# Optimization experiments

Hardware: AMD Instinct MI355X
Metric: run time of the kernel (lower is better)

The kernel has to match this reference:

```python
import jax, jax.numpy as jnp
import numpy as np

N_NODES = 500000


def _gconv(x, src, dst, ew, w_neigh, b, w_self):
    # DGL GraphConv(norm='none'): multiply weight first (in>=out here), then aggregate.
    h = x @ w_neigh                      # [N, out]
    msg = h[src] * ew[:, None]           # [E, out]
    agg = jax.ops.segment_sum(msg, dst, num_segments=N_NODES)
    return agg + b + x @ w_self          # neigh conv (+bias) + self-loop linear (no bias)


def setup_inputs() -> dict:
    key = jax.random.key(0)
    ks = jax.random.split(key, 16)
    N, E, G, F = N_NODES, 16000000, 64, 16
    inp = {
        "x": jax.random.normal(ks[0], (N, F), jnp.float32),
        "src": jax.random.randint(ks[1], (E,), 0, N),
        "dst": jax.random.randint(ks[2], (E,), 0, N),
        "graph_id": jnp.sort(jax.random.randint(ks[3], (N,), 0, G)),
        "edge_weight": jax.random.uniform(ks[4], (E,), jnp.float32),
        "num_graphs": G,
        "w_neigh0": jax.random.normal(ks[5], (F, 1), jnp.float32),
        "b0": jax.random.normal(ks[6], (1,), jnp.float32),
        "w_self0": jax.random.normal(ks[7], (F, 1), jnp.float32),
        "w_neigh1": jax.random.normal(ks[8], (1, 1), jnp.float32),
        "b1": jax.random.normal(ks[9], (1,), jnp.float32),
        "w_self1": jax.random.normal(ks[10], (1, 1), jnp.float32),
        "w_neigh2": jax.random.normal(ks[11], (1, 1), jnp.float32),
        "b2": jax.random.normal(ks[12], (1,), jnp.float32),
        "w_self2": jax.random.normal(ks[13], (1, 1), jnp.float32),
        "fc1_w": jax.random.normal(ks[14], (8, 1), jnp.float32),
        "fc1_b": jax.random.normal(ks[15], (8,), jnp.float32),
        "out_w": jax.random.normal(jax.random.fold_in(key, 100), (4, 8), jnp.float32),
        "out_b": jax.random.normal(jax.random.fold_in(key, 101), (4,), jnp.float32),
    }
    return inp


def reference(x, src, dst, graph_id, edge_weight, num_graphs,
              w_neigh0, b0, w_self0, w_neigh1, b1, w_self1,
              w_neigh2, b2, w_self2, fc1_w, fc1_b, out_w, out_b):
    h = jax.nn.relu(_gconv(x, src, dst, edge_weight, w_neigh0, b0, w_self0))
    h = jax.nn.relu(_gconv(h, src, dst, edge_weight, w_neigh1, b1, w_self1))
    h = jax.nn.relu(_gconv(h, src, dst, edge_weight, w_neigh2, b2, w_self2))
    # dgl.sum_nodes: per-graph segment sum over batched graph -> [G, 1]
    hg = jax.ops.segment_sum(h, graph_id, num_segments=num_graphs)
    hg2 = jax.nn.sigmoid((hg @ fc1_w.T + fc1_b) * 1000.0)   # [G, 8]
    out = jax.nn.relu(hg2 @ out_w.T + out_b)                # [G, 4]
    return jax.nn.log_softmax(out, axis=1)
```

## Files before the change

kernel.cpp:

```cpp
#include <hip/hip_runtime.h>

#define N_NODES   500000
#define NGRAPH    64
#define FDIM      16
#define NPB       4096
#define NPB_SHIFT 12
#define NBINS     123
#define SLICES    4
#define NBLK      512
#define CH        4096
typedef unsigned int u32;
typedef unsigned long long u64;

__global__ void proj_kernel(const float* __restrict__ x,
                            const float* __restrict__ wn,
                            const float* __restrict__ wsf,
                            float* __restrict__ a,
                            float* __restrict__ s) {
    int i = blockIdx.x * blockDim.x + threadIdx.x;
    if (i >= N_NODES) return;
    const float4* xr = (const float4*)(x + (size_t)i * FDIM);
    float4 v0 = xr[0], v1 = xr[1], v2 = xr[2], v3 = xr[3];
    const float4* n4 = (const float4*)wn;
    const float4* s4 = (const float4*)wsf;
    float4 n0 = n4[0], n1 = n4[1], n2 = n4[2], n3 = n4[3];
    float4 w0 = s4[0], w1 = s4[1], w2 = s4[2], w3 = s4[3];
    float an = v0.x*n0.x + v0.y*n0.y + v0.z*n0.z + v0.w*n0.w
             + v1.x*n1.x + v1.y*n1.y + v1.z*n1.z + v1.w*n1.w
             + v2.x*n2.x + v2.y*n2.y + v2.z*n2.z + v2.w*n2.w
             + v3.x*n3.x + v3.y*n3.y + v3.z*n3.z + v3.w*n3.w;
    float as = v0.x*w0.x + v0.y*w0.y + v0.z*w0.z + v0.w*w0.w
             + v1.x*w1.x + v1.y*w1.y + v1.z*w1.z + v1.w*w1.w
             + v2.x*w2.x + v2.y*w2.y + v2.z*w2.z + v2.w*w2.w
             + v3.x*w3.x + v3.y*w3.y + v3.z*w3.z + v3.w*w3.w;
    a[i] = an;
    s[i] = as;
}

__global__ __launch_bounds__(1024) void hist_kernel(const int* __restrict__ dst, int E, int chunk,
                                                    u32* __restrict__ blockHist) {
    __shared__ u32 cnt[NBINS];
    for (int t = threadIdx.x; t < NBINS; t += 1024) cnt[t] = 0;
    __syncthreads();
    int b = blockIdx.x;
    int lo = b * chunk, hi = min(lo + chunk, E);
    int m = (hi - lo) & ~3;
    for (int i = lo + threadIdx.x * 4; i < lo + m; i += 4096) {
        int4 d = *(const int4*)(dst + i);
        atomicAdd(&cnt[((u32)d.x) >> NPB_SHIFT], 1u);
        atomicAdd(&cnt[((u32)d.y) >> NPB_SHIFT], 1u);
        atomicAdd(&cnt[((u32)d.z) >> NPB_SHIFT], 1u);
        atomicAdd(&cnt[((u32)d.w) >> NPB_SHIFT], 1u);
    }
    for (int i = lo + m + threadIdx.x; i < hi; i += 1024)
        atomicAdd(&cnt[((u32)dst[i]) >> NPB_SHIFT], 1u);
    __syncthreads();
    for (int t = threadIdx.x; t < NBINS; t += 1024)
        blockHist[(size_t)b * NBINS + t] = cnt[t];
}

__global__ __launch_bounds__(NBLK) void scan1_kernel(u32* __restrict__ blockHist,
                                                     u32* __restrict__ binTotal) {
    int j = blockIdx.x;
    __shared__ u32 lsum[NBLK];
    int t = threadIdx.x;
    u32 v = blockHist[(size_t)t * NBINS + j];
    lsum[t] = v;
    __syncthreads();
    u32 x = v;
    for (int off = 1; off < NBLK; off <<= 1) {
        u32 y = (t >= off) ? lsum[t - off] : 0u;
        __syncthreads();
        x += y; lsum[t] = x;
        __syncthreads();
    }
    if (t == NBLK - 1) binTotal[j] = x;
    blockHist[(size_t)t * NBINS + j] = x - v;
}

__global__ void scan2_kernel(const u32* __restrict__ binTotal, u32* __restrict__ binStart) {
    if (threadIdx.x == 0) {
        u32 run = 0;
        for (int j = 0; j < NBINS; ++j) { binStart[j] = run; run += binTotal[j]; }
        binStart[NBINS] = run;
    }
}

__global__ __launch_bounds__(512) void scatter_staged(const int* __restrict__ src,
                                                      const int* __restrict__ dst,
                                                      const float* __restrict__ ew,
                                                      int E, int chunk,
                                                      const u32* __restrict__ blockHist,
                                                      const u32* __restrict__ binStart,
                                                      u64* __restrict__ binned) {
    __shared__ u32 cursor[NBINS];
    __shared__ u32 cnt[NBINS];
    __shared__ u32 off[NBINS];
    __shared__ u64 stage[CH];
    __shared__ unsigned char binOf[CH];
    int b   = blockIdx.x;
    int tid = threadIdx.x;
    for (int t = tid; t < NBINS; t += 512)
        cursor[t] = binStart[t] + blockHist[(size_t)b * NBINS + t];
    int lo = b * chunk, hiB = min(lo + chunk, E);
    for (int base = lo; base < hiB; base += CH) {
        int n = min(CH, hiB - base);
        for (int t = tid; t < NBINS; t += 512) cnt[t] = 0;
        __syncthreads();
        u32 rec[8]; float wv[8]; u32 bi[8]; u32 rk[8];
#pragma unroll
        for (int k = 0; k < 8; ++k) {
            int idx = base + k * 512 + tid;
            bi[k] = 0xFFFFFFFFu;
            if (idx < base + n) {
                u32 d  = (u32)dst[idx];
                bi[k]  = d >> NPB_SHIFT;
                rec[k] = ((u32)src[idx]) | ((d & (NPB - 1)) << 19);
                wv[k]  = ew[idx];
                rk[k]  = atomicAdd(&cnt[bi[k]], 1u);
            }
        }
        __syncthreads();
        if (tid < NBINS) off[tid] = cnt[tid];
        __syncthreads();
        for (int d2 = 1; d2 < 128; d2 <<= 1) {
            u32 v = 0;
            if (tid < NBINS) { v = off[tid]; if (tid >= d2) v += off[tid - d2]; }
            __syncthreads();
            if (tid < NBINS) off[tid] = v;
            __syncthreads();
        }
        if (tid < NBINS) off[tid] -= cnt[tid];
        __syncthreads();
#pragma unroll
        for (int k = 0; k < 8; ++k) {
            if (bi[k] != 0xFFFFFFFFu) {
                u32 p = off[bi[k]] + rk[k];
                stage[p] = (u64)rec[k] | ((u64)__float_as_uint(wv[k]) << 32);
                binOf[p] = (unsigned char)bi[k];
            }
        }
        __syncthreads();
        for (int p = tid; p < n; p += 512) {
            u32 j = binOf[p];
            binned[cursor[j] + ((u32)p - off[j])] = stage[p];
        }
        __syncthreads();
        for (int t = tid; t < NBINS; t += 512) cursor[t] += cnt[t];
        __syncthreads();
    }
}

__global__ __launch_bounds__(512) void bin_pass(const u64* __restrict__ binned,
                                                const u32* __restrict__ binStart,
                                                const float* __restrict__ hsrc,
                                                float* __restrict__ partials) {
    __shared__ float acc[NPB];
    int blk   = blockIdx.x;
    int j     = blk >> 2;
    int slice = blk & (SLICES - 1);
    for (int t = threadIdx.x; t < NPB; t += 512) acc[t] = 0.0f;
    __syncthreads();
    u32 blo = binStart[j], bhi = binStart[j + 1];
    u32 cnt = bhi - blo;
    u32 per = (cnt + SLICES - 1) / SLICES;
    u32 lo = blo + slice * per;
    u32 hi = min(lo + per, bhi);

    u32 i = lo + threadIdx.x;
    for (; i + 7u * 512u < hi; i += 8u * 512u) {
        u64 e[8];
#pragma unroll
        for (int k = 0; k < 8; ++k) e[k] = __builtin_nontemporal_load(&binned[i + (u32)k * 512u]);
        float g[8];
#pragma unroll
        for (int k = 0; k < 8; ++k) g[k] = hsrc[((u32)e[k]) & 0x7FFFFu];
#pragma unroll
        for (int k = 0; k < 8; ++k)
            atomicAdd(&acc[((u32)e[k]) >> 19], g[k] * __uint_as_float((u32)(e[k] >> 32)));
    }
    for (; i < hi; i += 512) {
        u64 e = __builtin_nontemporal_load(&binned[i]);
        u32 xx = (u32)e;
        atomicAdd(&acc[xx >> 19], hsrc[xx & 0x7FFFFu] * __uint_as_float((u32)(e >> 32)));
    }
    __syncthreads();
    float* p = partials + (size_t)(j * SLICES + slice) * NPB;
    for (int t = threadIdx.x; t < NPB; t += 512)
        __builtin_nontemporal_store(acc[t], &p[t]);
}

__global__ void merge_update(const float* __restrict__ partials,
                             const float* __restrict__ selfv,
                             const float* __restrict__ wnp,
                             const float* __restrict__ bp,
                             const float* __restrict__ wsp,
                             float* __restrict__ hout) {
    int n = blockIdx.x * blockDim.x + threadIdx.x;
    if (n >= N_NODES) return;
    int j = n >> NPB_SHIFT;
    int l = n & (NPB - 1);
    const float* p = partials + (size_t)j * SLICES * NPB + l;
    float sum = p[0] + p[NPB] + p[2 * NPB] + p[3 * NPB];
    float scale = wnp ? wnp[0] : 1.0f;
    float wself = wsp ? wsp[0] : 1.0f;
    hout[n] = fmaxf(sum * scale + bp[0] + selfv[n] * wself, 0.0f);
}

__global__ void edge_pass(const int* __restrict__ src, const int* __restrict__ dst,
                          const float* __restrict__ ew, const float* __restrict__ h,
                          float* __restrict__ agg, const float* __restrict__ wnp, int E) {
    float scale = wnp ? wnp[0] : 1.0f;
    int stride = gridDim.x * blockDim.x;
    for (int i = blockIdx.x * blockDim.x + threadIdx.x; i < E; i += stride)
        atomicAdd(&agg[dst[i]], h[src[i]] * ew[i] * scale);
}
__global__ void node_update(const float* __restrict__ agg, const float* __restrict__ selfv,
                            const float* __restrict__ bp, const float* __restrict__ wsp,
                            float* __restrict__ hout) {
    int i = blockIdx.x * blockDim.x + threadIdx.x;
    if (i >= N_NODES) return;
    float wsc = wsp ? wsp[0] : 1.0f;
    hout[i] = fmaxf(agg[i] + bp[0] + selfv[i] * wsc, 0.0f);
}

__global__ void graph_sum(const float* __restrict__ h, const int* __restrict__ gid,
                          float* __restrict__ hg) {
    __shared__ float loc[NGRAPH];
    int t = threadIdx.x;
    if (t < NGRAPH) loc[t] = 0.0f;
    __syncthreads();
    int stride = gridDim.x * blockDim.x;
    for (int i = blockIdx.x * blockDim.x + t; i < N_NODES; i += stride)
        atomicAdd(&loc[gid[i]], h[i]);
    __syncthreads();
    if (t < NGRAPH) atomicAdd(&hg[t], loc[t]);
}

__global__ void head_kernel(const float* __restrict__ hg,
                            const float* __restrict__ fc1w, const float* __restrict__ fc1b,
                            const float* __restrict__ outw, const float* __restrict__ outb,
                            float* __restrict__ out) {
    int g = threadIdx.x;
    if (g >= NGRAPH) return;
    float v = hg[g];
    float t[8];
#pragma unroll
    for (int j = 0; j < 8; ++j) {
        float z = (v * fc1w[j] + fc1b[j]) * 1000.0f;
        t[j] = 1.0f / (1.0f + expf(-z));
    }
    float o[4];
#pragma unroll
    for (int k = 0; k < 4; ++k) {
        float acc2 = outb[k];
#pragma unroll
        for (int j = 0; j < 8; ++j) acc2 += t[j] * outw[k * 8 + j];
        o[k] = fmaxf(acc2, 0.0f);
    }
    float m = fmaxf(fmaxf(o[0], o[1]), fmaxf(o[2], o[3]));
    float se = 0.0f;
#pragma unroll
    for (int k = 0; k < 4; ++k) se += expf(o[k] - m);
    float lse = m + logf(se);
#pragma unroll
    for (int k = 0; k < 4; ++k) out[g * 4 + k] = o[k] - lse;
}

extern "C" void kernel_launch(void* const* d_in, const int* in_sizes, int n_in,
                              void* d_out, int out_size, void* d_ws, size_t ws_size,
                              hipStream_t stream) {
    const float* x    = (const float*)d_in[0];
    const int*   src  = (const int*)  d_in[1];
    const int*   dst  = (const int*)  d_in[2];
    const int*   gid  = (const int*)  d_in[3];
    const float* ew   = (const float*)d_in[4];
    const float* wn0  = (const float*)d_in[6];
    const float* b0   = (const float*)d_in[7];
    const float* ws0  = (const float*)d_in[8];
    const float* wn1  = (const float*)d_in[9];
    const float* b1   = (const float*)d_in[10];
    const float* ws1  = (const float*)d_in[11];
    const float* wn2  = (const float*)d_in[12];
    const float* b2   = (const float*)d_in[13];
    const float* ws2  = (const float*)d_in[14];
    const float* fc1w = (const float*)d_in[15];
    const float* fc1b = (const float*)d_in[16];
    const float* outw = (const float*)d_in[17];
    const float* outb = (const float*)d_in[18];
    int E = in_sizes[1];

    const int BLK = 256;
    int nodeGrid = (N_NODES + BLK - 1) / BLK;
    char* ws = (char*)d_ws;

    size_t off = 0;
    u64*   binned    = (u64*)(ws + off);   off += (size_t)E * 8;
    u32*   blockHist = (u32*)(ws + off);   off += (size_t)NBLK * NBINS * 4;
    u32*   binStart  = (u32*)(ws + off);   off += (NBINS + 1) * 4;
    off = (off + 63) & ~(size_t)63;
    u32*   binTotal  = (u32*)(ws + off);   off += (NBINS + 1) * 4;
    off = (off + 63) & ~(size_t)63;
    float* partials  = (float*)(ws + off); off += (size_t)NBINS * SLICES * NPB * 4;
    float* a  = (float*)(ws + off); off += (size_t)N_NODES * 4;
    float* s  = (float*)(ws + off); off += (size_t)N_NODES * 4;
    float* h0 = (float*)(ws + off); off += (size_t)N_NODES * 4;
    float* h1 = (float*)(ws + off); off += (size_t)N_NODES * 4;
    float* hg = (float*)(ws + off); off += NGRAPH * 4;
    size_t need = off;

    if (ws_size >= need) {
        int chunk = (((E + NBLK - 1) / NBLK) + 3) & ~3;

        proj_kernel<<<nodeGrid, BLK, 0, stream>>>(x, wn0, ws0, a, s);

        hist_kernel<<<NBLK, 1024, 0, stream>>>(dst, E, chunk, blockHist);
        scan1_kernel<<<NBINS, NBLK, 0, stream>>>(blockHist, binTotal);
        scan2_kernel<<<1, 64, 0, stream>>>(binTotal, binStart);
        scatter_staged<<<NBLK, 512, 0, stream>>>(src, dst, ew, E, chunk, blockHist, binStart, binned);

        bin_pass<<<NBINS * SLICES, 512, 0, stream>>>(binned, binStart, a, partials);
        merge_update<<<nodeGrid, BLK, 0, stream>>>(partials, s, nullptr, b0, nullptr, h0);
        bin_pass<<<NBINS * SLICES, 512, 0, stream>>>(binned, binStart, h0, partials);
        merge_update<<<nodeGrid, BLK, 0, stream>>>(partials, h0, wn1, b1, ws1, h1);
        bin_pass<<<NBINS * SLICES, 512, 0, stream>>>(binned, binStart, h1, partials);
        merge_update<<<nodeGrid, BLK, 0, stream>>>(partials, h1, wn2, b2, ws2, a);

        (void)hipMemsetAsync(hg, 0, NGRAPH * sizeof(float), stream);
        graph_sum<<<512, BLK, 0, stream>>>(a, gid, hg);
        head_kernel<<<1, 64, 0, stream>>>(hg, fc1w, fc1b, outw, outb, (float*)d_out);
    } else {
        float* wsb  = (float*)d_ws;
        float* fa   = wsb;
        float* fs   = wsb + 1 * (size_t)N_NODES;
        float* fagg = wsb + 2 * (size_t)N_NODES;
        float* fh   = wsb + 3 * (size_t)N_NODES;
        float* fhg  = wsb + 4 * (size_t)N_NODES;

        proj_kernel<<<nodeGrid, BLK, 0, stream>>>(x, wn0, ws0, fa, fs);

        (void)hipMemsetAsync(fagg, 0, (size_t)N_NODES * sizeof(float), stream);
        edge_pass<<<4096, BLK, 0, stream>>>(src, dst, ew, fa, fagg, nullptr, E);
        node_update<<<nodeGrid, BLK, 0, stream>>>(fagg, fs, b0, nullptr, fh);

        (void)hipMemsetAsync(fagg, 0, (size_t)N_NODES * sizeof(float), stream);
        edge_pass<<<4096, BLK, 0, stream>>>(src, dst, ew, fh, fagg, wn1, E);
        node_update<<<nodeGrid, BLK, 0, stream>>>(fagg, fh, b1, ws1, fh);

        (void)hipMemsetAsync(fagg, 0, (size_t)N_NODES * sizeof(float), stream);
        edge_pass<<<4096, BLK, 0, stream>>>(src, dst, ew, fh, fagg, wn2, E);
        node_update<<<nodeGrid, BLK, 0, stream>>>(fagg, fh, b2, ws2, fh);

        (void)hipMemsetAsync(fhg, 0, NGRAPH * sizeof(float), stream);
        graph_sum<<<512, BLK, 0, stream>>>(fh, gid, fhg);
        head_kernel<<<1, 64, 0, stream>>>(fhg, fc1w, fc1b, outw, outb, (float*)d_out);
    }
}
```

Measured before the change: 424.2 us.

## Fuse projection into histogram, raise block and slice counts, vectorize graph sum

Merges the node projection into the histogram kernel as extra blocks so both run in one launch. Doubles the histogram/scatter block count and, when workspace allows, splits each bin across 8 slices instead of 4 in the aggregation passes. It also parallelizes the bin-start scan and makes the per-graph sum use vectorized loads with wave-level reductions when a wavefront's nodes share a graph. The aim is more parallelism and fewer launches, at the cost of more partial buffers to merge and larger scan workloads.

```diff
diff --git a/kernel.cpp b/kernel.cpp
--- a/kernel.cpp
+++ b/kernel.cpp
@@ -6,57 +6,57 @@
 #define NPB       4096
 #define NPB_SHIFT 12
 #define NBINS     123
-#define SLICES    4
-#define NBLK      512
+#define NBLK      1024
 #define CH        4096
 typedef unsigned int u32;
 typedef unsigned long long u64;
 
-__global__ void proj_kernel(const float* __restrict__ x,
-                            const float* __restrict__ wn,
-                            const float* __restrict__ wsf,
-                            float* __restrict__ a,
-                            float* __restrict__ s) {
-    int i = blockIdx.x * blockDim.x + threadIdx.x;
-    if (i >= N_NODES) return;
-    const float4* xr = (const float4*)(x + (size_t)i * FDIM);
-    float4 v0 = xr[0], v1 = xr[1], v2 = xr[2], v3 = xr[3];
-    const float4* n4 = (const float4*)wn;
-    const float4* s4 = (const float4*)wsf;
-    float4 n0 = n4[0], n1 = n4[1], n2 = n4[2], n3 = n4[3];
-    float4 w0 = s4[0], w1 = s4[1], w2 = s4[2], w3 = s4[3];
-    float an = v0.x*n0.x + v0.y*n0.y + v0.z*n0.z + v0.w*n0.w
-             + v1.x*n1.x + v1.y*n1.y + v1.z*n1.z + v1.w*n1.w
-             + v2.x*n2.x + v2.y*n2.y + v2.z*n2.z + v2.w*n2.w
-             + v3.x*n3.x + v3.y*n3.y + v3.z*n3.z + v3.w*n3.w;
-    float as = v0.x*w0.x + v0.y*w0.y + v0.z*w0.z + v0.w*w0.w
-             + v1.x*w1.x + v1.y*w1.y + v1.z*w1.z + v1.w*w1.w
-             + v2.x*w2.x + v2.y*w2.y + v2.z*w2.z + v2.w*w2.w
-             + v3.x*w3.x + v3.y*w3.y + v3.z*w3.z + v3.w*w3.w;
-    a[i] = an;
-    s[i] = as;
-}
-
-__global__ __launch_bounds__(1024) void hist_kernel(const int* __restrict__ dst, int E, int chunk,
-                                                    u32* __restrict__ blockHist) {
+__global__ __launch_bounds__(1024) void proj_hist(const int* __restrict__ dst, int E, int chunk,
+                                                  u32* __restrict__ blockHist,
+                                                  const float* __restrict__ x,
+                                                  const float* __restrict__ wn,
+                                                  const float* __restrict__ wsf,
+                                                  float* __restrict__ a,
+                                                  float* __restrict__ s) {
     __shared__ u32 cnt[NBINS];
-    for (int t = threadIdx.x; t < NBINS; t += 1024) cnt[t] = 0;
-    __syncthreads();
-    int b = blockIdx.x;
-    int lo = b * chunk, hi = min(lo + chunk, E);
-    int m = (hi - lo) & ~3;
-    for (int i = lo + threadIdx.x * 4; i < lo + m; i += 4096) {
-        int4 d = *(const int4*)(dst + i);
-        atomicAdd(&cnt[((u32)d.x) >> NPB_SHIFT], 1u);
-        atomicAdd(&cnt[((u32)d.y) >> NPB_SHIFT], 1u);
-        atomicAdd(&cnt[((u32)d.z) >> NPB_SHIFT], 1u);
-        atomicAdd(&cnt[((u32)d.w) >> NPB_SHIFT], 1u);
-    }
-    for (int i = lo + m + threadIdx.x; i < hi; i += 1024)
-        atomicAdd(&cnt[((u32)dst[i]) >> NPB_SHIFT], 1u);
-    __syncthreads();
-    for (int t = threadIdx.x; t < NBINS; t += 1024)
-        blockHist[(size_t)b * NBINS + t] = cnt[t];
+    if (blockIdx.x < NBLK) {
+        for (int t = threadIdx.x; t < NBINS; t += 1024) cnt[t] = 0;
+        __syncthreads();
+        int b = blockIdx.x;
+        int lo = b * chunk, hi = min(lo + chunk, E);
+        int m = (hi - lo) & ~3;
+        for (int i = lo + threadIdx.x * 4; i < lo + m; i += 4096) {
+            int4 d = *(const int4*)(dst + i);
+            atomicAdd(&cnt[((u32)d.x) >> NPB_SHIFT], 1u);
+            atomicAdd(&cnt[((u32)d.y) >> NPB_SHIFT], 1u);
+            atomicAdd(&cnt[((u32)d.z) >> NPB_SHIFT], 1u);
+            atomicAdd(&cnt[((u32)d.w) >> NPB_SHIFT], 1u);
+        }
+        for (int i = lo + m + threadIdx.x; i < hi; i += 1024)
+            atomicAdd(&cnt[((u32)dst[i]) >> NPB_SHIFT], 1u);
+        __syncthreads();
+        for (int t = threadIdx.x; t < NBINS; t += 1024)
+            blockHist[(size_t)b * NBINS + t] = cnt[t];
+    } else {
+        int i = (blockIdx.x - NBLK) * 1024 + threadIdx.x;
+        if (i >= N_NODES) return;
+        const float4* xr = (const float4*)(x + (size_t)i * FDIM);
+        float4 v0 = xr[0], v1 = xr[1], v2 = xr[2], v3 = xr[3];
+        const float4* n4 = (const float4*)wn;
+        const float4* s4 = (const float4*)wsf;
+        float4 n0 = n4[0], n1 = n4[1], n2 = n4[2], n3 = n4[3];
+        float4 w0 = s4[0], w1 = s4[1], w2 = s4[2], w3 = s4[3];
+        float an = v0.x*n0.x + v0.y*n0.y + v0.z*n0.z + v0.w*n0.w
+                 + v1.x*n1.x + v1.y*n1.y + v1.z*n1.z + v1.w*n1.w
+                 + v2.x*n2.x + v2.y*n2.y + v2.z*n2.z + v2.w*n2.w
+                 + v3.x*n3.x + v3.y*n3.y + v3.z*n3.z + v3.w*n3.w;
+        float as = v0.x*w0.x + v0.y*w0.y + v0.z*w0.z + v0.w*w0.w
+                 + v1.x*w1.x + v1.y*w1.y + v1.z*w1.z + v1.w*w1.w
+                 + v2.x*w2.x + v2.y*w2.y + v2.z*w2.z + v2.w*w2.w
+                 + v3.x*w3.x + v3.y*w3.y + v3.z*w3.z + v3.w*w3.w;
+        a[i] = an;
+        s[i] = as;
+    }
 }
 
 __global__ __launch_bounds__(NBLK) void scan1_kernel(u32* __restrict__ blockHist,
@@ -79,11 +79,19 @@
 }
 
 __global__ void scan2_kernel(const u32* __restrict__ binTotal, u32* __restrict__ binStart) {
-    if (threadIdx.x == 0) {
-        u32 run = 0;
-        for (int j = 0; j < NBINS; ++j) { binStart[j] = run; run += binTotal[j]; }
-        binStart[NBINS] = run;
-    }
+    __shared__ u32 sh[128];
+    int t = threadIdx.x;
+    u32 v = (t < NBINS) ? binTotal[t] : 0u;
+    sh[t] = v;
+    __syncthreads();
+    for (int d = 1; d < 128; d <<= 1) {
+        u32 y = (t >= d) ? sh[t - d] : 0u;
+        __syncthreads();
+        sh[t] += y;
+        __syncthreads();
+    }
+    if (t < NBINS) binStart[t] = sh[t] - v;
+    if (t == 127) binStart[NBINS] = sh[127];
 }
 
 __global__ __launch_bounds__(512) void scatter_staged(const int* __restrict__ src,
@@ -151,19 +159,20 @@
     }
 }
 
+template<int S>
 __global__ __launch_bounds__(512) void bin_pass(const u64* __restrict__ binned,
                                                 const u32* __restrict__ binStart,
                                                 const float* __restrict__ hsrc,
                                                 float* __restrict__ partials) {
     __shared__ float acc[NPB];
     int blk   = blockIdx.x;
-    int j     = blk >> 2;
-    int slice = blk & (SLICES - 1);
+    int j     = blk / S;
+    int slice = blk % S;
     for (int t = threadIdx.x; t < NPB; t += 512) acc[t] = 0.0f;
     __syncthreads();
     u32 blo = binStart[j], bhi = binStart[j + 1];
     u32 cnt = bhi - blo;
-    u32 per = (cnt + SLICES - 1) / SLICES;
+    u32 per = (cnt + S - 1) / S;
     u32 lo = blo + slice * per;
     u32 hi = min(lo + per, bhi);
 
@@ -185,11 +194,12 @@
         atomicAdd(&acc[xx >> 19], hsrc[xx & 0x7FFFFu] * __uint_as_float((u32)(e >> 32)));
     }
     __syncthreads();
-    float* p = partials + (size_t)(j * SLICES + slice) * NPB;
+    float* p = partials + (size_t)(j * S + slice) * NPB;
     for (int t = threadIdx.x; t < NPB; t += 512)
         __builtin_nontemporal_store(acc[t], &p[t]);
 }
 
+template<int S>
 __global__ void merge_update(const float* __restrict__ partials,
                              const float* __restrict__ selfv,
                              const float* __restrict__ wnp,
@@ -200,8 +210,10 @@
     if (n >= N_NODES) return;
     int j = n >> NPB_SHIFT;
     int l = n & (NPB - 1);
-    const float* p = partials + (size_t)j * SLICES * NPB + l;
-    float sum = p[0] + p[NPB] + p[2 * NPB] + p[3 * NPB];
+    const float* p = partials + (size_t)j * S * NPB + l;
+    float sum = 0.0f;
+#pragma unroll
+    for (int k = 0; k < S; ++k) sum += __builtin_nontemporal_load(&p[k * NPB]);
     float scale = wnp ? wnp[0] : 1.0f;
     float wself = wsp ? wsp[0] : 1.0f;
     hout[n] = fmaxf(sum * scale + bp[0] + selfv[n] * wself, 0.0f);
@@ -223,16 +235,45 @@
     float wsc = wsp ? wsp[0] : 1.0f;
     hout[i] = fmaxf(agg[i] + bp[0] + selfv[i] * wsc, 0.0f);
 }
-
-__global__ void graph_sum(const float* __restrict__ h, const int* __restrict__ gid,
-                          float* __restrict__ hg) {
+__global__ void proj_kernel(const float* __restrict__ x, const float* __restrict__ wn,
+                            const float* __restrict__ wsf, float* __restrict__ a,
+                            float* __restrict__ s) {
+    int i = blockIdx.x * blockDim.x + threadIdx.x;
+    if (i >= N_NODES) return;
+    float an = 0.f, as = 0.f;
+    for (int k = 0; k < FDIM; ++k) {
+        float v = x[(size_t)i * FDIM + k];
+        an += v * wn[k]; as += v * wsf[k];
+    }
+    a[i] = an; s[i] = as;
+}
+
+__global__ __launch_bounds__(256) void graph_sum(const float* __restrict__ h,
+                                                 const int* __restrict__ gid,
+                                                 float* __restrict__ hg) {
     __shared__ float loc[NGRAPH];
     int t = threadIdx.x;
     if (t < NGRAPH) loc[t] = 0.0f;
     __syncthreads();
+    int nq = N_NODES / 4;
     int stride = gridDim.x * blockDim.x;
-    for (int i = blockIdx.x * blockDim.x + t; i < N_NODES; i += stride)
-        atomicAdd(&loc[gid[i]], h[i]);
+    for (int q = blockIdx.x * blockDim.x + t; q < nq; q += stride) {
+        int4   g4 = *(const int4*)(gid + 4 * q);
+        float4 h4 = *(const float4*)(h + 4 * q);
+        int g0 = __shfl(g4.x, 0);
+        bool uni = (g4.x == g0) & (g4.w == g0);
+        if (__all(uni)) {
+            float v = h4.x + h4.y + h4.z + h4.w;
+#pragma unroll
+            for (int o = 32; o > 0; o >>= 1) v += __shfl_down(v, o);
+            if ((t & 63) == 0) atomicAdd(&loc[g0], v);
+        } else {
+            atomicAdd(&loc[g4.x], h4.x);
+            atomicAdd(&loc[g4.y], h4.y);
+            atomicAdd(&loc[g4.z], h4.z);
+            atomicAdd(&loc[g4.w], h4.w);
+        }
+    }
     __syncthreads();
     if (t < NGRAPH) atomicAdd(&hg[t], loc[t]);
 }
@@ -301,33 +342,49 @@
     off = (off + 63) & ~(size_t)63;
     u32*   binTotal  = (u32*)(ws + off);   off += (NBINS + 1) * 4;
     off = (off + 63) & ~(size_t)63;
-    float* partials  = (float*)(ws + off); off += (size_t)NBINS * SLICES * NPB * 4;
-    float* a  = (float*)(ws + off); off += (size_t)N_NODES * 4;
-    float* s  = (float*)(ws + off); off += (size_t)N_NODES * 4;
-    float* h0 = (float*)(ws + off); off += (size_t)N_NODES * 4;
-    float* h1 = (float*)(ws + off); off += (size_t)N_NODES * 4;
-    float* hg = (float*)(ws + off); off += NGRAPH * 4;
-    size_t need = off;
-
-    if (ws_size >= need) {
+    float* partials  = (float*)(ws + off);
+    size_t base_off  = off;
+    size_t nodes_bytes = 4 * (size_t)N_NODES * 4 + NGRAPH * 4;
+    size_t need8 = base_off + (size_t)NBINS * 8 * NPB * 4 + nodes_bytes;
+    size_t need4 = base_off + (size_t)NBINS * 4 * NPB * 4 + nodes_bytes;
+
+    int S = (ws_size >= need8) ? 8 : ((ws_size >= need4) ? 4 : 0);
+
+    if (S) {
+        off = base_off + (size_t)NBINS * S * NPB * 4;
+        float* a  = (float*)(ws + off); off += (size_t)N_NODES * 4;
+        float* s  = (float*)(ws + off); off += (size_t)N_NODES * 4;
+        float* h0 = (float*)(ws + off); off += (size_t)N_NODES * 4;
+        float* h1 = (float*)(ws + off); off += (size_t)N_NODES * 4;
+        float* hg = (float*)(ws + off);
+
         int chunk = (((E + NBLK - 1) / NBLK) + 3) & ~3;
-
-        proj_kernel<<<nodeGrid, BLK, 0, stream>>>(x, wn0, ws0, a, s);
-
-        hist_kernel<<<NBLK, 1024, 0, stream>>>(dst, E, chunk, blockHist);
+        int projBlocks = (N_NODES + 1023) / 1024;
+
+        proj_hist<<<NBLK + projBlocks, 1024, 0, stream>>>(dst, E, chunk, blockHist,
+                                                          x, wn0, ws0, a, s);
         scan1_kernel<<<NBINS, NBLK, 0, stream>>>(blockHist, binTotal);
-        scan2_kernel<<<1, 64, 0, stream>>>(binTotal, binStart);
+        scan2_kernel<<<1, 128, 0, stream>>>(binTotal, binStart);
         scatter_staged<<<NBLK, 512, 0, stream>>>(src, dst, ew, E, chunk, blockHist, binStart, binned);
 
-        bin_pass<<<NBINS * SLICES, 512, 0, stream>>>(binned, binStart, a, partials);
-        merge_update<<<nodeGrid, BLK, 0, stream>>>(partials, s, nullptr, b0, nullptr, h0);
-        bin_pass<<<NBINS * SLICES, 512, 0, stream>>>(binned, binStart, h0, partials);
-        merge_update<<<nodeGrid, BLK, 0, stream>>>(partials, h0, wn1, b1, ws1, h1);
-        bin_pass<<<NBINS * SLICES, 512, 0, stream>>>(binned, binStart, h1, partials);
-        merge_update<<<nodeGrid, BLK, 0, stream>>>(partials, h1, wn2, b2, ws2, a);
+        if (S == 8) {
+            bin_pass<8><<<NBINS * 8, 512, 0, stream>>>(binned, binStart, a, partials);
+            merge_update<8><<<nodeGrid, BLK, 0, stream>>>(partials, s, nullptr, b0, nullptr, h0);
+            bin_pass<8><<<NBINS * 8, 512, 0, stream>>>(binned, binStart, h0, partials);
+            merge_update<8><<<nodeGrid, BLK, 0, stream>>>(partials, h0, wn1, b1, ws1, h1);
+            bin_pass<8><<<NBINS * 8, 512, 0, stream>>>(binned, binStart, h1, partials);
+            merge_update<8><<<nodeGrid, BLK, 0, stream>>>(partials, h1, wn2, b2, ws2, a);
+        } else {
+            bin_pass<4><<<NBINS * 4, 512, 0, stream>>>(binned, binStart, a, partials);
+            merge_update<4><<<nodeGrid, BLK, 0, stream>>>(partials, s, nullptr, b0, nullptr, h0);
+            bin_pass<4><<<NBINS * 4, 512, 0, stream>>>(binned, binStart, h0, partials);
+            merge_update<4><<<nodeGrid, BLK, 0, stream>>>(partials, h0, wn1, b1, ws1, h1);
+            bin_pass<4><<<NBINS * 4, 512, 0, stream>>>(binned, binStart, h1, partials);
+            merge_update<4><<<nodeGrid, BLK, 0, stream>>>(partials, h1, wn2, b2, ws2, a);
+        }
 
         (void)hipMemsetAsync(hg, 0, NGRAPH * sizeof(float), stream);
-        graph_sum<<<512, BLK, 0, stream>>>(a, gid, hg);
+        graph_sum<<<512, 256, 0, stream>>>(a, gid, hg);
         head_kernel<<<1, 64, 0, stream>>>(hg, fc1w, fc1b, outw, outb, (float*)d_out);
     } else {
         float* wsb  = (float*)d_ws;
@@ -352,7 +409,7 @@
         node_update<<<nodeGrid, BLK, 0, stream>>>(fagg, fh, b2, ws2, fh);
 
         (void)hipMemsetAsync(fhg, 0, NGRAPH * sizeof(float), stream);
-        graph_sum<<<512, BLK, 0, stream>>>(fh, gid, fhg);
+        graph_sum<<<512, 256, 0, stream>>>(fh, gid, fhg);
         head_kernel<<<1, 64, 0, stream>>>(fhg, fc1w, fc1b, outw, outb, (float*)d_out);
     }
 }
```

Measured after the change: 408.6 us. 1.04x faster.
